# Kernel optimization log

Hardware: AMD Instinct MI355X
Metric: run time of the kernel (lower is better)

## Reference

```python
import jax, jax.numpy as jnp
import numpy as np

E = 768           # EMBEDDING_DIM
L = 768           # LATENT_DIM
H = 12            # ATTENTION_HEAD_COUNT
HD = L // H       # head_dim = 64
EPS = 1e-5


def _linear_params(key, fan_in, fan_out):
    kw, kb = jax.random.split(key)
    bound = 1.0 / np.sqrt(fan_in)
    w = jax.random.uniform(kw, (fan_in, fan_out), jnp.float32, -bound, bound)
    b = jax.random.uniform(kb, (fan_out,), jnp.float32, -bound, bound)
    return w, b


def layer_norm(x, g, b):
    m = jnp.mean(x, axis=-1, keepdims=True)
    v = jnp.mean((x - m) ** 2, axis=-1, keepdims=True)
    return (x - m) * jax.lax.rsqrt(v + EPS) * g + b


def setup_inputs() -> dict:
    key = jax.random.key(0)
    ks = jax.random.split(key, 8)
    B, N, M = 8, 1024, 1024
    x = jax.random.normal(ks[0], (B, N, E), jnp.float32)
    y = jax.random.normal(ks[1], (B, M, E), jnp.float32)
    wq, bq = _linear_params(ks[2], E, L)
    wk, bk = _linear_params(ks[3], E, L)
    wv, bv = _linear_params(ks[4], E, E * H)
    w_in, b_in = _linear_params(ks[5], E, L)
    w_out, b_out = _linear_params(ks[6], L, E)
    ones = jnp.ones((E,), jnp.float32)
    zeros = jnp.zeros((E,), jnp.float32)
    return {
        'x': x, 'y': y,
        'ln1_g': ones, 'ln1_b': zeros,
        'ln2_g': ones, 'ln2_b': zeros,
        'ln3_g': ones, 'ln3_b': zeros,
        'wq': wq, 'bq': bq,
        'wk': wk, 'bk': bk,
        'wv': wv, 'bv': bv,
        'w_in': w_in, 'b_in': b_in,
        'w_out': w_out, 'b_out': b_out,
    }


def reference(x, y, ln1_g, ln1_b, ln2_g, ln2_b, ln3_g, ln3_b,
              wq, bq, wk, bk, wv, bv, w_in, b_in, w_out, b_out):
    B, N, _ = x.shape
    M = y.shape[1]
    xn = layer_norm(x, ln1_g, ln1_b)
    yn = layer_norm(y, ln2_g, ln2_b)
    # projections; per-head value dim is the FULL embedding dim (non-standard)
    q = (xn @ wq + bq).reshape(B, N, H, HD)        # bnhd
    k = (yn @ wk + bk).reshape(B, M, H, HD)        # bmhd
    v = (yn @ wv + bv).reshape(B, M, H, E)         # bmhe
    a = jnp.einsum('bnhd,bmhd->bhnm', q, k) / jnp.sqrt(jnp.float32(HD))
    a = jax.nn.softmax(a, axis=-1)
    # attention output fused with the sum over heads (heads summed, not concat)
    dx = jnp.einsum('bhnm,bmhe->bne', a, v)
    h = xn + dx
    h = layer_norm(h, ln3_g, ln3_b)
    mlp = jax.nn.relu(h @ w_in + b_in) @ w_out + b_out
    return (h + mlp, yn)
```

## Files before the change

kernel.cpp:

```cpp
#include <hip/hip_runtime.h>
#include <hip/hip_bf16.h>
#include <stdint.h>

typedef __bf16 bf16_t;
typedef __bf16 bf16x8 __attribute__((ext_vector_type(8)));
typedef float  f32x4  __attribute__((ext_vector_type(4)));

typedef __attribute__((address_space(3))) unsigned int lds_u32;
typedef const __attribute__((address_space(1))) unsigned int glob_u32;
#define GLDS16(g, l) __builtin_amdgcn_global_load_lds((glob_u32*)(g), (lds_u32*)(l), 16, 0, 0)

__device__ __forceinline__ f32x4 mfma16(bf16x8 a, bf16x8 b, f32x4 c) {
    return __builtin_amdgcn_mfma_f32_16x16x32_bf16(a, b, c, 0, 0, 0);
}

__device__ __forceinline__ float ldv(const void* p, long i, int fp32mode) {
    return fp32mode ? ((const float*)p)[i] : (float)((const bf16_t*)p)[i];
}

__global__ __launch_bounds__(256)
void detect_dtype(const void* __restrict__ x, int* __restrict__ flag) {
    __shared__ int cnt;
    if (threadIdx.x == 0) cnt = 0;
    __syncthreads();
    const bf16_t* p = (const bf16_t*)x;
    int local = 0;
    for (int i = threadIdx.x; i < 4096; i += 256) {
        const float v = (float)p[i];
        if (!(fabsf(v) < 1e6f)) local++;
    }
    atomicAdd(&cnt, local);
    __syncthreads();
    if (threadIdx.x == 0) { flag[0] = (cnt >= 16) ? 1 : 0; flag[1] = 0; }
}

__global__ __launch_bounds__(256)
void transpose_cvt(const void* __restrict__ in, bf16_t* __restrict__ out,
                   int R, int C, const int* __restrict__ flagp) {
    __shared__ bf16_t t[32][33];
    const int mode = *flagp;
    const long zi = (long)blockIdx.z * R * C;
    const int c0 = blockIdx.x * 32;
    const int r0 = blockIdx.y * 32;
    const int x  = threadIdx.x;
    const int y0 = threadIdx.y;
    for (int yy = y0; yy < 32; yy += 8)
        t[yy][x] = (bf16_t)ldv(in, zi + (long)(r0 + yy) * C + c0 + x, mode);
    __syncthreads();
    for (int yy = y0; yy < 32; yy += 8)
        out[zi + (long)(c0 + yy) * R + r0 + x] = t[x][yy];
}

__global__ __launch_bounds__(256)
void transpose_wv(const void* __restrict__ in, bf16_t* __restrict__ out,
                  const int* __restrict__ flagp) {
    __shared__ bf16_t t[32][33];
    const int mode = *flagp;
    const int h  = blockIdx.z;
    const int e0 = blockIdx.x * 32;
    const int k0 = blockIdx.y * 32;
    const int x  = threadIdx.x;
    const int y0 = threadIdx.y;
    for (int yy = y0; yy < 32; yy += 8)
        t[yy][x] = (bf16_t)ldv(in, (long)(k0 + yy) * 9216 + h * 768 + e0 + x, mode);
    __syncthreads();
    for (int yy = y0; yy < 32; yy += 8)
        out[(long)(e0 + yy) * 9216 + h * 768 + k0 + x] = t[x][yy];
}

__global__ __launch_bounds__(256)
void bvsum_k(const void* __restrict__ bv, float* __restrict__ out,
             const int* __restrict__ flagp) {
    const int mode = *flagp;
    const int e = blockIdx.x * 256 + threadIdx.x;
    if (e < 768) {
        float s = 0.f;
#pragma unroll
        for (int h = 0; h < 12; ++h) s += ldv(bv, h * 768 + e, mode);
        out[e] = s;
    }
}

__global__ __launch_bounds__(256)
void ln768(const void* __restrict__ in, bf16_t* __restrict__ out,
           const void* __restrict__ gam, const void* __restrict__ bet,
           const int* __restrict__ dmodep, const int* __restrict__ pmodep) {
    __shared__ float rs[256], rq[256];
    const int dm = *dmodep, pm = *pmodep;
    const long base = (long)blockIdx.x * 768;
    const int tid = threadIdx.x;
    float v[3];
    float s = 0.f, q = 0.f;
#pragma unroll
    for (int i = 0; i < 3; ++i) {
        v[i] = ldv(in, base + i * 256 + tid, dm);
        s += v[i];
        q += v[i] * v[i];
    }
    rs[tid] = s; rq[tid] = q;
    __syncthreads();
    for (int st = 128; st > 0; st >>= 1) {
        if (tid < st) { rs[tid] += rs[tid + st]; rq[tid] += rq[tid + st]; }
        __syncthreads();
    }
    const float mean = rs[0] * (1.0f / 768.0f);
    const float var  = rq[0] * (1.0f / 768.0f) - mean * mean;
    const float rstd = rsqrtf(var + 1e-5f);
#pragma unroll
    for (int i = 0; i < 3; ++i) {
        const int c = i * 256 + tid;
        out[base + c] = (bf16_t)((v[i] - mean) * rstd * ldv(gam, c, pm) + ldv(bet, c, pm));
    }
}

#define BK 64
#define TILEA 16384

template<int JN>
__device__ __forceinline__ void stage_ab(const bf16_t* Az, const bf16_t* Bz,
                                         int lda, int ldb, int k0,
                                         char* lA, char* lB, int tid) {
    const int srow = tid >> 3;
    const int sc   = ((tid & 7) * 16) ^ ((srow & 7) << 4);
#pragma unroll
    for (int p = 0; p < 4; ++p)
        GLDS16((const char*)(Az + (long)(srow + p * 32) * lda + k0) + sc, lA + p * 4096);
#pragma unroll
    for (int p = 0; p < JN; ++p)
        GLDS16((const char*)(Bz + (long)(srow + p * 32) * ldb + k0) + sc, lB + p * 4096);
}

template<int JN>
__device__ __forceinline__ void compute_tile(const char* As, const char* Bs,
                                             int wm, int wn, int l15, int quad,
                                             f32x4 (&acc)[4][JN]) {
#pragma unroll
    for (int kk = 0; kk < BK; kk += 32) {
        bf16x8 af[4], bfr[JN];
        const int cb = kk * 2 + quad * 16;
#pragma unroll
        for (int i = 0; i < 4; ++i) {
            const int r = wm + i * 16 + l15;
            af[i] = *(const bf16x8*)(As + r * 128 + (cb ^ ((r & 7) << 4)));
        }
#pragma unroll
        for (int j = 0; j < JN; ++j) {
            const int r = wn + j * 16 + l15;
            bfr[j] = *(const bf16x8*)(Bs + r * 128 + (cb ^ ((r & 7) << 4)));
        }
#pragma unroll
        for (int i = 0; i < 4; ++i)
#pragma unroll
            for (int j = 0; j < JN; ++j)
                acc[i][j] = mfma16(af[i], bfr[j], acc[i][j]);
    }
}

template<int JN>
__device__ __forceinline__ void kloop(const bf16_t* Az, const bf16_t* Bz,
                                      int K, int lda, int ldb, int tid,
                                      char* AsB, char* BsB,
                                      int wm, int wn, int l15, int quad,
                                      f32x4 (&acc)[4][JN]) {
    const int TILEB = JN * 4096;
    char* lA = AsB + (tid >> 6) * 1024;
    char* lB = BsB + (tid >> 6) * 1024;
    int cur = 0;
    stage_ab<JN>(Az, Bz, lda, ldb, 0, lA, lB, tid);
    __syncthreads();
    const int NT = K >> 6;
    for (int t = 0; t < NT - 1; ++t) {
        const int nb = cur ^ 1;
        stage_ab<JN>(Az, Bz, lda, ldb, (t + 1) << 6, lA + nb * TILEA, lB + nb * TILEB, tid);
        compute_tile<JN>(AsB + cur * TILEA, BsB + cur * TILEB, wm, wn, l15, quad, acc);
        __syncthreads();
        cur = nb;
    }
    compute_tile<JN>(AsB + cur * TILEA, BsB + cur * TILEB, wm, wn, l15, quad, acc);
}

__device__ __forceinline__ int xcd_swz(int lin, int nwg) {
    return (lin & 7) * (nwg >> 3) + (lin >> 3);
}

__global__ __launch_bounds__(256, 2)
void gemm_bt(const bf16_t* __restrict__ A, const bf16_t* __restrict__ B,
             bf16_t* __restrict__ C,
             int K, int lda, int ldb, int ldc,
             const void* __restrict__ bias, const int* __restrict__ flagp,
             const bf16_t* __restrict__ res, int do_relu) {
    __shared__ char AsB[2 * TILEA];
    __shared__ char BsB[2 * 3 * 4096];
    const int bmode = *flagp;
    const int swz = xcd_swz(blockIdx.y * 8 + blockIdx.x, 512);
    const int n0 = (swz & 7) * 96;
    const int m0 = (swz >> 3) * 128;
    const bf16_t* Az = A + (long)m0 * lda;
    const bf16_t* Bz = B + (long)n0 * ldb;

    const int tid  = threadIdx.x;
    const int lane = tid & 63;
    const int w    = tid >> 6;
    const int wm   = (w >> 1) * 64;
    const int wn   = (w & 1) * 48;
    const int l15  = lane & 15;
    const int quad = lane >> 4;

    const f32x4 fz = {0.f, 0.f, 0.f, 0.f};
    f32x4 acc[4][3];
#pragma unroll
    for (int i = 0; i < 4; ++i)
#pragma unroll
        for (int j = 0; j < 3; ++j) acc[i][j] = fz;

    kloop<3>(Az, Bz, K, lda, ldb, tid, AsB, BsB, wm, wn, l15, quad, acc);

#pragma unroll
    for (int i = 0; i < 4; ++i) {
#pragma unroll
        for (int j = 0; j < 3; ++j) {
            const int mb = m0 + wm + i * 16 + quad * 4;
            const int nc = n0 + wn + j * 16 + l15;
#pragma unroll
            for (int r = 0; r < 4; ++r) {
                float v = acc[i][j][r];
                if (bias) v += ldv(bias, nc, bmode);
                if (do_relu) v = fmaxf(v, 0.0f);
                if (res) v += (float)res[(long)(mb + r) * ldc + nc];
                C[(long)(mb + r) * ldc + nc] = (bf16_t)v;
            }
        }
    }
}

__global__ __launch_bounds__(256, 2)
void gemm_qk(const bf16_t* __restrict__ xn, const bf16_t* __restrict__ ynb,
             const bf16_t* __restrict__ wqT, const bf16_t* __restrict__ wkT,
             bf16_t* __restrict__ qb, bf16_t* __restrict__ kb,
             const void* __restrict__ bq, const void* __restrict__ bk,
             const int* __restrict__ flagp) {
    __shared__ char AsB[2 * TILEA];
    __shared__ char BsB[2 * 3 * 4096];
    const int bmode = *flagp;
    const int z = blockIdx.z;
    const bf16_t* A = z ? ynb : xn;
    const bf16_t* B = z ? wkT : wqT;
    bf16_t*       C = z ? kb  : qb;
    const void* bias = z ? bk : bq;
    const int swz = xcd_swz(blockIdx.y * 8 + blockIdx.x, 512);
    const int n0 = (swz & 7) * 96;
    const int m0 = (swz >> 3) * 128;
    const bf16_t* Az = A + (long)m0 * 768;
    const bf16_t* Bz = B + (long)n0 * 768;

    const int tid  = threadIdx.x;
    const int lane = tid & 63;
    const int w    = tid >> 6;
    const int wm   = (w >> 1) * 64;
    const int wn   = (w & 1) * 48;
    const int l15  = lane & 15;
    const int quad = lane >> 4;

    const f32x4 fz = {0.f, 0.f, 0.f, 0.f};
    f32x4 acc[4][3];
#pragma unroll
    for (int i = 0; i < 4; ++i)
#pragma unroll
        for (int j = 0; j < 3; ++j) acc[i][j] = fz;

    kloop<3>(Az, Bz, 768, 768, 768, tid, AsB, BsB, wm, wn, l15, quad, acc);

#pragma unroll
    for (int i = 0; i < 4; ++i) {
#pragma unroll
        for (int j = 0; j < 3; ++j) {
            const int mb = m0 + wm + i * 16 + quad * 4;
            const int nc = n0 + wn + j * 16 + l15;
#pragma unroll
            for (int r = 0; r < 4; ++r)
                C[(long)(mb + r) * 768 + nc] = (bf16_t)(acc[i][j][r] + ldv(bias, nc, bmode));
        }
    }
}

__global__ __launch_bounds__(256, 2)
void gemm_vt(const bf16_t* __restrict__ W2T, const bf16_t* __restrict__ ynb,
             bf16_t* __restrict__ VTc, int h0, int ldP) {
    __shared__ char AsB[2 * TILEA];
    __shared__ char BsB[2 * 4 * 4096];
    const int L  = blockIdx.z * 48 + blockIdx.y * 8 + blockIdx.x;
    const int b  = L & 7;
    const int rest = L >> 3;
    const int hc = rest / 48;
    const int t  = rest % 48;
    const int e0  = (t >> 3) * 128;
    const int mc0 = (t & 7) * 128;
    const bf16_t* Az = W2T + (long)e0 * 9216 + (h0 + hc) * 768;
    const bf16_t* Bz = ynb + ((long)b * 1024 + mc0) * 768;

    const int tid  = threadIdx.x;
    const int lane = tid & 63;
    const int w    = tid >> 6;
    const int wm   = (w >> 1) * 64;
    const int wn   = (w & 1) * 64;
    const int l15  = lane & 15;
    const int quad = lane >> 4;

    const f32x4 fz = {0.f, 0.f, 0.f, 0.f};
    f32x4 acc[4][4];
#pragma unroll
    for (int i = 0; i < 4; ++i)
#pragma unroll
        for (int j = 0; j < 4; ++j) acc[i][j] = fz;

    kloop<4>(Az, Bz, 768, 9216, 768, tid, AsB, BsB, wm, wn, l15, quad, acc);

    bf16_t* C = VTc + (long)b * 768 * ldP + (long)hc * 1024;
#pragma unroll
    for (int i = 0; i < 4; ++i) {
#pragma unroll
        for (int j = 0; j < 4; ++j) {
            const int er = e0 + wm + i * 16 + quad * 4;
            const int mc = mc0 + wn + j * 16 + l15;
#pragma unroll
            for (int r = 0; r < 4; ++r)
                C[(long)(er + r) * ldP + mc] = (bf16_t)acc[i][j][r];
        }
    }
}

__global__ __launch_bounds__(256, 2)
void gemm_dx(const bf16_t* __restrict__ P, const bf16_t* __restrict__ VTc,
             float* __restrict__ dxf, const bf16_t* __restrict__ xnb,
             const float* __restrict__ bvs, bf16_t* __restrict__ hp,
             int ldP, int mode) {
    __shared__ char AsB[2 * TILEA];
    __shared__ char BsB[2 * 3 * 4096];
    const int L = blockIdx.z * 64 + blockIdx.y * 8 + blockIdx.x;
    const int b = L & 7;
    const int t = L >> 3;
    const int m0 = (t >> 3) * 128;
    const int n0 = (t & 7) * 96;
    const bf16_t* Az = P   + ((long)b * 1024 + m0) * ldP;
    const bf16_t* Bz = VTc + ((long)b * 768  + n0) * ldP;

    const int tid  = threadIdx.x;
    const int lane = tid & 63;
    const int w    = tid >> 6;
    const int wm   = (w >> 1) * 64;
    const int wn   = (w & 1) * 48;
    const int l15  = lane & 15;
    const int quad = lane >> 4;

    const f32x4 fz = {0.f, 0.f, 0.f, 0.f};
    f32x4 acc[4][3];
#pragma unroll
    for (int i = 0; i < 4; ++i)
#pragma unroll
        for (int j = 0; j < 3; ++j) acc[i][j] = fz;

    kloop<3>(Az, Bz, ldP, ldP, ldP, tid, AsB, BsB, wm, wn, l15, quad, acc);

#pragma unroll
    for (int i = 0; i < 4; ++i) {
#pragma unroll
        for (int j = 0; j < 3; ++j) {
            const int gr = b * 1024 + m0 + wm + i * 16 + quad * 4;
            const int nc = n0 + wn + j * 16 + l15;
#pragma unroll
            for (int r = 0; r < 4; ++r) {
                const long gi = (long)(gr + r) * 768 + nc;
                float v = acc[i][j][r];
                if (mode == 1 || mode == 2) v += dxf[gi];
                if (mode <= 1) dxf[gi] = v;
                else hp[gi] = (bf16_t)(v + bvs[nc] + (float)xnb[gi]);
            }
        }
    }
}

__global__ __launch_bounds__(512, 8)
void fused_S(const bf16_t* __restrict__ Q, const bf16_t* __restrict__ Kp,
             bf16_t* __restrict__ P, int h0, int ldP) {
    __shared__ bf16_t Pl[16][1032];
    __shared__ float  rmax[8][16];
    __shared__ float  rsum[8][16];

    const int bx   = blockIdx.x;
    const int b    = bx & 7;
    const int n0   = ((bx >> 3) & 63) * 16;
    const int hc   = bx >> 9;
    const int h    = h0 + hc;
    const int tid  = threadIdx.x;
    const int w    = tid >> 6;
    const int lane = tid & 63;
    const int l15  = lane & 15;
    const int quad = lane >> 4;

    const f32x4 fz = {0.f, 0.f, 0.f, 0.f};
    const long qoff = (long)(b * 1024 + n0 + l15) * 768 + h * 64 + quad * 8;
    const long koff = (long)(b * 1024) * 768 + h * 64 + quad * 8;

    f32x4 s[8];
#pragma unroll
    for (int f = 0; f < 8; ++f) s[f] = fz;
    const bf16x8 qa0 = *(const bf16x8*)(Q + qoff);
    const bf16x8 qa1 = *(const bf16x8*)(Q + qoff + 32);
#pragma unroll
    for (int f = 0; f < 8; ++f) {
        const int m = w * 128 + f * 16 + l15;
        const bf16_t* kp = Kp + koff + (long)m * 768;
        s[f] = mfma16(qa0, *(const bf16x8*)kp, s[f]);
        s[f] = mfma16(qa1, *(const bf16x8*)(kp + 32), s[f]);
    }
    float rm[4] = {-3e38f, -3e38f, -3e38f, -3e38f};
#pragma unroll
    for (int f = 0; f < 8; ++f)
#pragma unroll
        for (int r = 0; r < 4; ++r) {
            s[f][r] *= 0.125f;
            rm[r] = fmaxf(rm[r], s[f][r]);
        }
#pragma unroll
    for (int off = 1; off < 16; off <<= 1)
#pragma unroll
        for (int r = 0; r < 4; ++r) rm[r] = fmaxf(rm[r], __shfl_xor(rm[r], off));
    if (l15 == 0) {
#pragma unroll
        for (int r = 0; r < 4; ++r) rmax[w][quad * 4 + r] = rm[r];
    }
    __syncthreads();
    float gm[4];
#pragma unroll
    for (int r = 0; r < 4; ++r) {
        float mx = rmax[0][quad * 4 + r];
#pragma unroll
        for (int w2 = 1; w2 < 8; ++w2) mx = fmaxf(mx, rmax[w2][quad * 4 + r]);
        gm[r] = mx;
    }
    float ps[4] = {0.f, 0.f, 0.f, 0.f};
#pragma unroll
    for (int f = 0; f < 8; ++f)
#pragma unroll
        for (int r = 0; r < 4; ++r) {
            const float p = __expf(s[f][r] - gm[r]);
            s[f][r] = p;
            ps[r] += p;
        }
#pragma unroll
    for (int off = 1; off < 16; off <<= 1)
#pragma unroll
        for (int r = 0; r < 4; ++r) ps[r] += __shfl_xor(ps[r], off);
    if (l15 == 0) {
#pragma unroll
        for (int r = 0; r < 4; ++r) rsum[w][quad * 4 + r] = ps[r];
    }
    __syncthreads();
#pragma unroll
    for (int r = 0; r < 4; ++r) {
        float ss = 0.f;
#pragma unroll
        for (int w2 = 0; w2 < 8; ++w2) ss += rsum[w2][quad * 4 + r];
        gm[r] = 1.0f / ss;
    }
#pragma unroll
    for (int f = 0; f < 8; ++f)
#pragma unroll
        for (int r = 0; r < 4; ++r)
            Pl[quad * 4 + r][w * 128 + f * 16 + l15] = (bf16_t)(s[f][r] * gm[r]);
    __syncthreads();

    const long pbase = ((long)b * 1024 + n0) * ldP + (long)hc * 1024;
    const int rr = tid >> 5;
    const int c0 = (tid & 31) * 32;
    bf16_t* dst = P + pbase + (long)rr * ldP + c0;
#pragma unroll
    for (int u = 0; u < 4; ++u)
        *(bf16x8*)(dst + u * 8) = *(const bf16x8*)(&Pl[rr][c0 + u * 8]);
}

__global__ __launch_bounds__(256)
void emit2(const bf16_t* __restrict__ a, const bf16_t* __restrict__ b,
           void* __restrict__ out, const int* __restrict__ flagp) {
    const int mode = *flagp;
    const long n = 6291456;
    const long stride = (long)gridDim.x * blockDim.x;
    for (long i = (long)blockIdx.x * blockDim.x + threadIdx.x; i < 2 * n; i += stride) {
        const bf16_t v = (i < n) ? a[i] : b[i - n];
        if (mode) ((float*)out)[i] = (float)v;
        else      ((bf16_t*)out)[i] = v;
    }
}

extern "C" void kernel_launch(void* const* d_in, const int* in_sizes, int n_in,
                              void* d_out, int out_size, void* d_ws, size_t ws_size,
                              hipStream_t stream) {
    (void)in_sizes; (void)n_in; (void)out_size;

    const void* x    = d_in[0];
    const void* y    = d_in[1];
    const void* ln1g = d_in[2];
    const void* ln1b = d_in[3];
    const void* ln2g = d_in[4];
    const void* ln2b = d_in[5];
    const void* ln3g = d_in[6];
    const void* ln3b = d_in[7];
    const void* wq   = d_in[8];
    const void* bq   = d_in[9];
    const void* wk   = d_in[10];
    const void* bk   = d_in[11];
    const void* wv   = d_in[12];
    const void* bv   = d_in[13];
    const void* wi   = d_in[14];
    const void* bi   = d_in[15];
    const void* wo   = d_in[16];
    const void* bo   = d_in[17];

    char* ws = (char*)d_ws;
    bf16_t* xn    = (bf16_t*)(ws + 0);
    bf16_t* ynb   = (bf16_t*)(ws + 12582912);
    bf16_t* qb    = (bf16_t*)(ws + 25165824);
    bf16_t* kb    = (bf16_t*)(ws + 37748736);
    bf16_t* W2T   = (bf16_t*)(ws + 50331648);
    bf16_t* wqT   = (bf16_t*)(ws + 64487424);
    bf16_t* wkT   = (bf16_t*)(ws + 65667072);
    bf16_t* wiT   = (bf16_t*)(ws + 66846720);
    bf16_t* woT   = (bf16_t*)(ws + 68026368);
    float*  bvs   = (float*) (ws + 69206016);
    int*    flag  = (int*)   (ws + 69210112);
    float*  dxf   = (float*) (ws + 69214208);

    static const int GS[5] = {12, 6, 4, 3, 2};
    int G = 2;
    for (int i = 0; i < 5; ++i) {
        const unsigned long long need =
            94380032ULL + (unsigned long long)GS[i] * 29360128ULL;
        if (need <= (unsigned long long)ws_size) { G = GS[i]; break; }
    }
    const int ldP = G * 1024;
    bf16_t* Pcat = (bf16_t*)(ws + 94380032);
    bf16_t* VTc  = (bf16_t*)(ws + 94380032 + (size_t)G * 16777216);
    bf16_t* hpre = qb;
    bf16_t* hn   = kb;
    bf16_t* mid  = Pcat;
    bf16_t* res0 = xn;
    const int* F = flag;
    const int* Z = flag + 1;

    detect_dtype<<<1, 256, 0, stream>>>(x, flag);

    const dim3 tb(32, 8);
    transpose_cvt<<<dim3(24, 24, 1), tb, 0, stream>>>(wq, wqT, 768, 768, F);
    transpose_cvt<<<dim3(24, 24, 1), tb, 0, stream>>>(wk, wkT, 768, 768, F);
    transpose_cvt<<<dim3(24, 24, 1), tb, 0, stream>>>(wi, wiT, 768, 768, F);
    transpose_cvt<<<dim3(24, 24, 1), tb, 0, stream>>>(wo, woT, 768, 768, F);
    transpose_wv<<<dim3(24, 24, 12), tb, 0, stream>>>(wv, W2T, F);
    bvsum_k<<<3, 256, 0, stream>>>(bv, bvs, F);

    ln768<<<8192, 256, 0, stream>>>(x, xn, ln1g, ln1b, F, F);
    ln768<<<8192, 256, 0, stream>>>(y, ynb, ln2g, ln2b, F, F);

    gemm_qk<<<dim3(8, 64, 2), 256, 0, stream>>>(xn, ynb, wqT, wkT, qb, kb, bq, bk, F);

    const int npass = 12 / G;
    for (int p = 0; p < npass; ++p) {
        const int h0 = p * G;
        fused_S<<<512 * G, 512, 0, stream>>>(qb, kb, Pcat, h0, ldP);
        gemm_vt<<<dim3(8, 6, 8 * G), 256, 0, stream>>>(W2T, ynb, VTc, h0, ldP);
        const int mode = (npass == 1) ? 3 : (p == 0 ? 0 : (p == npass - 1 ? 2 : 1));
        gemm_dx<<<dim3(8, 8, 8), 256, 0, stream>>>(Pcat, VTc, dxf, xn, bvs, hpre,
                                                   ldP, mode);
    }

    ln768<<<8192, 256, 0, stream>>>(hpre, hn, ln3g, ln3b, Z, F);

    gemm_bt<<<dim3(8, 64), 256, 0, stream>>>(hn, wiT, mid, 768, 768, 768, 768,
                                             bi, F, nullptr, 1);
    gemm_bt<<<dim3(8, 64), 256, 0, stream>>>(mid, woT, res0, 768, 768, 768, 768,
                                             bo, F, hn, 0);

    emit2<<<2048, 256, 0, stream>>>(res0, ynb, d_out, F);
}
```

Before: 897.9 us.

## Enlarge GEMM block tiles to 512 threads with 8 waves per workgroup

All bf16 GEMM kernels (qk, vt, dx, MLP) move from 256-thread blocks to 512-thread blocks. Each block now covers a larger output tile: 128x192 for most kernels and 256x128 for gemm_vt. Staging is generalized to separate A/B row-pass counts and the grids and tile-index mappings are rewritten to match. The aim is more reuse of each LDS-staged tile and fewer global loads per output. The costs are fewer blocks, which can hurt load balance on a many-CU GPU, and roughly double the LDS per block, which may limit occupancy.

After: 913.3 us. No clear change (+1.7%).

```diff
diff --git a/kernel.cpp b/kernel.cpp
--- a/kernel.cpp
+++ b/kernel.cpp
@@ -114,29 +114,28 @@
 }
 
 #define BK 64
-#define TILEA 16384
-
-template<int JN>
+
+template<int AP, int BP>
 __device__ __forceinline__ void stage_ab(const bf16_t* Az, const bf16_t* Bz,
                                          int lda, int ldb, int k0,
                                          char* lA, char* lB, int tid) {
     const int srow = tid >> 3;
     const int sc   = ((tid & 7) * 16) ^ ((srow & 7) << 4);
 #pragma unroll
-    for (int p = 0; p < 4; ++p)
-        GLDS16((const char*)(Az + (long)(srow + p * 32) * lda + k0) + sc, lA + p * 4096);
-#pragma unroll
-    for (int p = 0; p < JN; ++p)
-        GLDS16((const char*)(Bz + (long)(srow + p * 32) * ldb + k0) + sc, lB + p * 4096);
-}
-
-template<int JN>
+    for (int p = 0; p < AP; ++p)
+        GLDS16((const char*)(Az + (long)(srow + p * 64) * lda + k0) + sc, lA + p * 8192);
+#pragma unroll
+    for (int p = 0; p < BP; ++p)
+        GLDS16((const char*)(Bz + (long)(srow + p * 64) * ldb + k0) + sc, lB + p * 8192);
+}
+
+template<int JNW>
 __device__ __forceinline__ void compute_tile(const char* As, const char* Bs,
                                              int wm, int wn, int l15, int quad,
-                                             f32x4 (&acc)[4][JN]) {
+                                             f32x4 (&acc)[4][JNW]) {
 #pragma unroll
     for (int kk = 0; kk < BK; kk += 32) {
-        bf16x8 af[4], bfr[JN];
+        bf16x8 af[4], bfr[JNW];
         const int cb = kk * 2 + quad * 16;
 #pragma unroll
         for (int i = 0; i < 4; ++i) {
@@ -144,65 +143,65 @@
             af[i] = *(const bf16x8*)(As + r * 128 + (cb ^ ((r & 7) << 4)));
         }
 #pragma unroll
-        for (int j = 0; j < JN; ++j) {
+        for (int j = 0; j < JNW; ++j) {
             const int r = wn + j * 16 + l15;
             bfr[j] = *(const bf16x8*)(Bs + r * 128 + (cb ^ ((r & 7) << 4)));
         }
 #pragma unroll
         for (int i = 0; i < 4; ++i)
 #pragma unroll
-            for (int j = 0; j < JN; ++j)
+            for (int j = 0; j < JNW; ++j)
                 acc[i][j] = mfma16(af[i], bfr[j], acc[i][j]);
     }
 }
 
-template<int JN>
+template<int JNW, int AP, int BP>
 __device__ __forceinline__ void kloop(const bf16_t* Az, const bf16_t* Bz,
                                       int K, int lda, int ldb, int tid,
                                       char* AsB, char* BsB,
                                       int wm, int wn, int l15, int quad,
-                                      f32x4 (&acc)[4][JN]) {
-    const int TILEB = JN * 4096;
+                                      f32x4 (&acc)[4][JNW]) {
+    const int TA = AP * 8192, TB = BP * 8192;
     char* lA = AsB + (tid >> 6) * 1024;
     char* lB = BsB + (tid >> 6) * 1024;
     int cur = 0;
-    stage_ab<JN>(Az, Bz, lda, ldb, 0, lA, lB, tid);
+    stage_ab<AP, BP>(Az, Bz, lda, ldb, 0, lA, lB, tid);
     __syncthreads();
     const int NT = K >> 6;
     for (int t = 0; t < NT - 1; ++t) {
         const int nb = cur ^ 1;
-        stage_ab<JN>(Az, Bz, lda, ldb, (t + 1) << 6, lA + nb * TILEA, lB + nb * TILEB, tid);
-        compute_tile<JN>(AsB + cur * TILEA, BsB + cur * TILEB, wm, wn, l15, quad, acc);
+        stage_ab<AP, BP>(Az, Bz, lda, ldb, (t + 1) << 6, lA + nb * TA, lB + nb * TB, tid);
+        compute_tile<JNW>(AsB + cur * TA, BsB + cur * TB, wm, wn, l15, quad, acc);
         __syncthreads();
         cur = nb;
     }
-    compute_tile<JN>(AsB + cur * TILEA, BsB + cur * TILEB, wm, wn, l15, quad, acc);
+    compute_tile<JNW>(AsB + cur * TA, BsB + cur * TB, wm, wn, l15, quad, acc);
 }
 
 __device__ __forceinline__ int xcd_swz(int lin, int nwg) {
     return (lin & 7) * (nwg >> 3) + (lin >> 3);
 }
 
-__global__ __launch_bounds__(256, 2)
+__global__ __launch_bounds__(512, 2)
 void gemm_bt(const bf16_t* __restrict__ A, const bf16_t* __restrict__ B,
              bf16_t* __restrict__ C,
              int K, int lda, int ldb, int ldc,
              const void* __restrict__ bias, const int* __restrict__ flagp,
              const bf16_t* __restrict__ res, int do_relu) {
-    __shared__ char AsB[2 * TILEA];
-    __shared__ char BsB[2 * 3 * 4096];
+    __shared__ char AsB[2 * 2 * 8192];
+    __shared__ char BsB[2 * 3 * 8192];
     const int bmode = *flagp;
-    const int swz = xcd_swz(blockIdx.y * 8 + blockIdx.x, 512);
-    const int n0 = (swz & 7) * 96;
-    const int m0 = (swz >> 3) * 128;
+    const int swz = xcd_swz(blockIdx.y * 4 + blockIdx.x, 256);
+    const int n0 = (swz & 3) * 192;
+    const int m0 = (swz >> 2) * 128;
     const bf16_t* Az = A + (long)m0 * lda;
     const bf16_t* Bz = B + (long)n0 * ldb;
 
     const int tid  = threadIdx.x;
     const int lane = tid & 63;
     const int w    = tid >> 6;
-    const int wm   = (w >> 1) * 64;
-    const int wn   = (w & 1) * 48;
+    const int wm   = (w >> 2) * 64;
+    const int wn   = (w & 3) * 48;
     const int l15  = lane & 15;
     const int quad = lane >> 4;
 
@@ -213,7 +212,7 @@
 #pragma unroll
         for (int j = 0; j < 3; ++j) acc[i][j] = fz;
 
-    kloop<3>(Az, Bz, K, lda, ldb, tid, AsB, BsB, wm, wn, l15, quad, acc);
+    kloop<3, 2, 3>(Az, Bz, K, lda, ldb, tid, AsB, BsB, wm, wn, l15, quad, acc);
 
 #pragma unroll
     for (int i = 0; i < 4; ++i) {
@@ -233,31 +232,31 @@
     }
 }
 
-__global__ __launch_bounds__(256, 2)
+__global__ __launch_bounds__(512, 2)
 void gemm_qk(const bf16_t* __restrict__ xn, const bf16_t* __restrict__ ynb,
              const bf16_t* __restrict__ wqT, const bf16_t* __restrict__ wkT,
              bf16_t* __restrict__ qb, bf16_t* __restrict__ kb,
              const void* __restrict__ bq, const void* __restrict__ bk,
              const int* __restrict__ flagp) {
-    __shared__ char AsB[2 * TILEA];
-    __shared__ char BsB[2 * 3 * 4096];
+    __shared__ char AsB[2 * 2 * 8192];
+    __shared__ char BsB[2 * 3 * 8192];
     const int bmode = *flagp;
     const int z = blockIdx.z;
     const bf16_t* A = z ? ynb : xn;
     const bf16_t* B = z ? wkT : wqT;
     bf16_t*       C = z ? kb  : qb;
     const void* bias = z ? bk : bq;
-    const int swz = xcd_swz(blockIdx.y * 8 + blockIdx.x, 512);
-    const int n0 = (swz & 7) * 96;
-    const int m0 = (swz >> 3) * 128;
+    const int swz = xcd_swz(blockIdx.y * 4 + blockIdx.x, 256);
+    const int n0 = (swz & 3) * 192;
+    const int m0 = (swz >> 2) * 128;
     const bf16_t* Az = A + (long)m0 * 768;
     const bf16_t* Bz = B + (long)n0 * 768;
 
     const int tid  = threadIdx.x;
     const int lane = tid & 63;
     const int w    = tid >> 6;
-    const int wm   = (w >> 1) * 64;
-    const int wn   = (w & 1) * 48;
+    const int wm   = (w >> 2) * 64;
+    const int wn   = (w & 3) * 48;
     const int l15  = lane & 15;
     const int quad = lane >> 4;
 
@@ -268,7 +267,7 @@
 #pragma unroll
         for (int j = 0; j < 3; ++j) acc[i][j] = fz;
 
-    kloop<3>(Az, Bz, 768, 768, 768, tid, AsB, BsB, wm, wn, l15, quad, acc);
+    kloop<3, 2, 3>(Az, Bz, 768, 768, 768, tid, AsB, BsB, wm, wn, l15, quad, acc);
 
 #pragma unroll
     for (int i = 0; i < 4; ++i) {
@@ -283,18 +282,15 @@
     }
 }
 
-__global__ __launch_bounds__(256, 2)
+__global__ __launch_bounds__(512, 2)
 void gemm_vt(const bf16_t* __restrict__ W2T, const bf16_t* __restrict__ ynb,
              bf16_t* __restrict__ VTc, int h0, int ldP) {
-    __shared__ char AsB[2 * TILEA];
-    __shared__ char BsB[2 * 4 * 4096];
-    const int L  = blockIdx.z * 48 + blockIdx.y * 8 + blockIdx.x;
-    const int b  = L & 7;
-    const int rest = L >> 3;
-    const int hc = rest / 48;
-    const int t  = rest % 48;
-    const int e0  = (t >> 3) * 128;
-    const int mc0 = (t & 7) * 128;
+    __shared__ char AsB[2 * 4 * 8192];
+    __shared__ char BsB[2 * 2 * 8192];
+    const int b   = blockIdx.x;
+    const int hc  = blockIdx.z;
+    const int e0  = (blockIdx.y >> 3) * 256;
+    const int mc0 = (blockIdx.y & 7) * 128;
     const bf16_t* Az = W2T + (long)e0 * 9216 + (h0 + hc) * 768;
     const bf16_t* Bz = ynb + ((long)b * 1024 + mc0) * 768;
 
@@ -313,7 +309,7 @@
 #pragma unroll
         for (int j = 0; j < 4; ++j) acc[i][j] = fz;
 
-    kloop<4>(Az, Bz, 768, 9216, 768, tid, AsB, BsB, wm, wn, l15, quad, acc);
+    kloop<4, 4, 2>(Az, Bz, 768, 9216, 768, tid, AsB, BsB, wm, wn, l15, quad, acc);
 
     bf16_t* C = VTc + (long)b * 768 * ldP + (long)hc * 1024;
 #pragma unroll
@@ -329,26 +325,25 @@
     }
 }
 
-__global__ __launch_bounds__(256, 2)
+__global__ __launch_bounds__(512, 2)
 void gemm_dx(const bf16_t* __restrict__ P, const bf16_t* __restrict__ VTc,
              float* __restrict__ dxf, const bf16_t* __restrict__ xnb,
              const float* __restrict__ bvs, bf16_t* __restrict__ hp,
              int ldP, int mode) {
-    __shared__ char AsB[2 * TILEA];
-    __shared__ char BsB[2 * 3 * 4096];
-    const int L = blockIdx.z * 64 + blockIdx.y * 8 + blockIdx.x;
-    const int b = L & 7;
-    const int t = L >> 3;
-    const int m0 = (t >> 3) * 128;
-    const int n0 = (t & 7) * 96;
+    __shared__ char AsB[2 * 2 * 8192];
+    __shared__ char BsB[2 * 3 * 8192];
+    const int b  = blockIdx.x;
+    const int t  = blockIdx.y;
+    const int m0 = (t >> 2) * 128;
+    const int n0 = (t & 3) * 192;
     const bf16_t* Az = P   + ((long)b * 1024 + m0) * ldP;
     const bf16_t* Bz = VTc + ((long)b * 768  + n0) * ldP;
 
     const int tid  = threadIdx.x;
     const int lane = tid & 63;
     const int w    = tid >> 6;
-    const int wm   = (w >> 1) * 64;
-    const int wn   = (w & 1) * 48;
+    const int wm   = (w >> 2) * 64;
+    const int wn   = (w & 3) * 48;
     const int l15  = lane & 15;
     const int quad = lane >> 4;
 
@@ -359,7 +354,7 @@
 #pragma unroll
         for (int j = 0; j < 3; ++j) acc[i][j] = fz;
 
-    kloop<3>(Az, Bz, ldP, ldP, ldP, tid, AsB, BsB, wm, wn, l15, quad, acc);
+    kloop<3, 2, 3>(Az, Bz, ldP, ldP, ldP, tid, AsB, BsB, wm, wn, l15, quad, acc);
 
 #pragma unroll
     for (int i = 0; i < 4; ++i) {
@@ -560,23 +555,23 @@
     ln768<<<8192, 256, 0, stream>>>(x, xn, ln1g, ln1b, F, F);
     ln768<<<8192, 256, 0, stream>>>(y, ynb, ln2g, ln2b, F, F);
 
-    gemm_qk<<<dim3(8, 64, 2), 256, 0, stream>>>(xn, ynb, wqT, wkT, qb, kb, bq, bk, F);
+    gemm_qk<<<dim3(4, 64, 2), 512, 0, stream>>>(xn, ynb, wqT, wkT, qb, kb, bq, bk, F);
 
     const int npass = 12 / G;
     for (int p = 0; p < npass; ++p) {
         const int h0 = p * G;
         fused_S<<<512 * G, 512, 0, stream>>>(qb, kb, Pcat, h0, ldP);
-        gemm_vt<<<dim3(8, 6, 8 * G), 256, 0, stream>>>(W2T, ynb, VTc, h0, ldP);
+        gemm_vt<<<dim3(8, 24, G), 512, 0, stream>>>(W2T, ynb, VTc, h0, ldP);
         const int mode = (npass == 1) ? 3 : (p == 0 ? 0 : (p == npass - 1 ? 2 : 1));
-        gemm_dx<<<dim3(8, 8, 8), 256, 0, stream>>>(Pcat, VTc, dxf, xn, bvs, hpre,
-                                                   ldP, mode);
+        gemm_dx<<<dim3(8, 32), 512, 0, stream>>>(Pcat, VTc, dxf, xn, bvs, hpre,
+                                                 ldP, mode);
     }
 
     ln768<<<8192, 256, 0, stream>>>(hpre, hn, ln3g, ln3b, Z, F);
 
-    gemm_bt<<<dim3(8, 64), 256, 0, stream>>>(hn, wiT, mid, 768, 768, 768, 768,
+    gemm_bt<<<dim3(4, 64), 512, 0, stream>>>(hn, wiT, mid, 768, 768, 768, 768,
                                              bi, F, nullptr, 1);
-    gemm_bt<<<dim3(8, 64), 256, 0, stream>>>(mid, woT, res0, 768, 768, 768, 768,
+    gemm_bt<<<dim3(4, 64), 512, 0, stream>>>(mid, woT, res0, 768, 768, 768, 768,
                                              bo, F, hn, 0);
 
     emit2<<<2048, 256, 0, stream>>>(res0, ynb, d_out, F);
```

## Replace async double-buffered GEMM k-loop with single-buffer padded LDS 128x128 tiles

Applied to the files above, without the earlier changes.

Swaps the global_load_lds double-buffered GEMM pipeline for a simpler register-staged single-buffer k-loop with padded LDS rows instead of XOR swizzle. Tiles grow from 128x96 to 128x128, grids and index math are adjusted for all GEMM kernels, and the occupancy hint is dropped. This raises per-block reuse and reduces block count, but loses overlap of loads with MFMA compute and adds an extra barrier per k-step.

Measured after the change: 949.1 us. +5.7%, slower.

```diff
diff --git a/kernel.cpp b/kernel.cpp
--- a/kernel.cpp
+++ b/kernel.cpp
@@ -5,10 +5,6 @@
 typedef __bf16 bf16_t;
 typedef __bf16 bf16x8 __attribute__((ext_vector_type(8)));
 typedef float  f32x4  __attribute__((ext_vector_type(4)));
-
-typedef __attribute__((address_space(3))) unsigned int lds_u32;
-typedef const __attribute__((address_space(1))) unsigned int glob_u32;
-#define GLDS16(g, l) __builtin_amdgcn_global_load_lds((glob_u32*)(g), (lds_u32*)(l), 16, 0, 0)
 
 __device__ __forceinline__ f32x4 mfma16(bf16x8 a, bf16x8 b, f32x4 c) {
     return __builtin_amdgcn_mfma_f32_16x16x32_bf16(a, b, c, 0, 0, 0);
@@ -113,88 +109,61 @@
     }
 }
 
+#define BM 128
+#define BN 128
 #define BK 64
-#define TILEA 16384
-
-template<int JN>
-__device__ __forceinline__ void stage_ab(const bf16_t* Az, const bf16_t* Bz,
-                                         int lda, int ldb, int k0,
-                                         char* lA, char* lB, int tid) {
+#define LDT 72
+
+__device__ __forceinline__ void r1_kloop(const bf16_t* Az, const bf16_t* Bz,
+                                         int K, int lda, int ldb, int tid,
+                                         bf16_t (*As)[LDT], bf16_t (*Bs)[LDT],
+                                         int wm, int wn, int l15, int quad,
+                                         f32x4 (&acc)[4][4]) {
     const int srow = tid >> 3;
-    const int sc   = ((tid & 7) * 16) ^ ((srow & 7) << 4);
-#pragma unroll
-    for (int p = 0; p < 4; ++p)
-        GLDS16((const char*)(Az + (long)(srow + p * 32) * lda + k0) + sc, lA + p * 4096);
-#pragma unroll
-    for (int p = 0; p < JN; ++p)
-        GLDS16((const char*)(Bz + (long)(srow + p * 32) * ldb + k0) + sc, lB + p * 4096);
-}
-
-template<int JN>
-__device__ __forceinline__ void compute_tile(const char* As, const char* Bs,
-                                             int wm, int wn, int l15, int quad,
-                                             f32x4 (&acc)[4][JN]) {
-#pragma unroll
-    for (int kk = 0; kk < BK; kk += 32) {
-        bf16x8 af[4], bfr[JN];
-        const int cb = kk * 2 + quad * 16;
-#pragma unroll
-        for (int i = 0; i < 4; ++i) {
-            const int r = wm + i * 16 + l15;
-            af[i] = *(const bf16x8*)(As + r * 128 + (cb ^ ((r & 7) << 4)));
-        }
-#pragma unroll
-        for (int j = 0; j < JN; ++j) {
-            const int r = wn + j * 16 + l15;
-            bfr[j] = *(const bf16x8*)(Bs + r * 128 + (cb ^ ((r & 7) << 4)));
-        }
-#pragma unroll
-        for (int i = 0; i < 4; ++i)
-#pragma unroll
-            for (int j = 0; j < JN; ++j)
-                acc[i][j] = mfma16(af[i], bfr[j], acc[i][j]);
-    }
-}
-
-template<int JN>
-__device__ __forceinline__ void kloop(const bf16_t* Az, const bf16_t* Bz,
-                                      int K, int lda, int ldb, int tid,
-                                      char* AsB, char* BsB,
-                                      int wm, int wn, int l15, int quad,
-                                      f32x4 (&acc)[4][JN]) {
-    const int TILEB = JN * 4096;
-    char* lA = AsB + (tid >> 6) * 1024;
-    char* lB = BsB + (tid >> 6) * 1024;
-    int cur = 0;
-    stage_ab<JN>(Az, Bz, lda, ldb, 0, lA, lB, tid);
-    __syncthreads();
-    const int NT = K >> 6;
-    for (int t = 0; t < NT - 1; ++t) {
-        const int nb = cur ^ 1;
-        stage_ab<JN>(Az, Bz, lda, ldb, (t + 1) << 6, lA + nb * TILEA, lB + nb * TILEB, tid);
-        compute_tile<JN>(AsB + cur * TILEA, BsB + cur * TILEB, wm, wn, l15, quad, acc);
+    const int scol = (tid & 7) * 8;
+    for (int k0 = 0; k0 < K; k0 += BK) {
         __syncthreads();
-        cur = nb;
-    }
-    compute_tile<JN>(AsB + cur * TILEA, BsB + cur * TILEB, wm, wn, l15, quad, acc);
+#pragma unroll
+        for (int p = 0; p < 4; ++p) {
+            const int r = srow + p * 32;
+            *(bf16x8*)(&As[r][scol]) = *(const bf16x8*)(Az + (long)r * lda + k0 + scol);
+            *(bf16x8*)(&Bs[r][scol]) = *(const bf16x8*)(Bz + (long)r * ldb + k0 + scol);
+        }
+        __syncthreads();
+#pragma unroll
+        for (int kk = 0; kk < BK; kk += 32) {
+            bf16x8 af[4], bfr[4];
+#pragma unroll
+            for (int i = 0; i < 4; ++i)
+                af[i] = *(const bf16x8*)(&As[wm + i * 16 + l15][kk + quad * 8]);
+#pragma unroll
+            for (int j = 0; j < 4; ++j)
+                bfr[j] = *(const bf16x8*)(&Bs[wn + j * 16 + l15][kk + quad * 8]);
+#pragma unroll
+            for (int i = 0; i < 4; ++i)
+#pragma unroll
+                for (int j = 0; j < 4; ++j)
+                    acc[i][j] = mfma16(af[i], bfr[j], acc[i][j]);
+        }
+    }
 }
 
 __device__ __forceinline__ int xcd_swz(int lin, int nwg) {
     return (lin & 7) * (nwg >> 3) + (lin >> 3);
 }
 
-__global__ __launch_bounds__(256, 2)
+__global__ __launch_bounds__(256)
 void gemm_bt(const bf16_t* __restrict__ A, const bf16_t* __restrict__ B,
              bf16_t* __restrict__ C,
              int K, int lda, int ldb, int ldc,
              const void* __restrict__ bias, const int* __restrict__ flagp,
              const bf16_t* __restrict__ res, int do_relu) {
-    __shared__ char AsB[2 * TILEA];
-    __shared__ char BsB[2 * 3 * 4096];
+    __shared__ bf16_t As[BM][LDT];
+    __shared__ bf16_t Bs[BN][LDT];
     const int bmode = *flagp;
-    const int swz = xcd_swz(blockIdx.y * 8 + blockIdx.x, 512);
-    const int n0 = (swz & 7) * 96;
-    const int m0 = (swz >> 3) * 128;
+    const int swz = xcd_swz(blockIdx.y * 6 + blockIdx.x, 384);
+    const int n0 = (swz % 6) * BN;
+    const int m0 = (swz / 6) * BM;
     const bf16_t* Az = A + (long)m0 * lda;
     const bf16_t* Bz = B + (long)n0 * ldb;
 
@@ -202,23 +171,23 @@
     const int lane = tid & 63;
     const int w    = tid >> 6;
     const int wm   = (w >> 1) * 64;
-    const int wn   = (w & 1) * 48;
+    const int wn   = (w & 1) * 64;
     const int l15  = lane & 15;
     const int quad = lane >> 4;
 
     const f32x4 fz = {0.f, 0.f, 0.f, 0.f};
-    f32x4 acc[4][3];
+    f32x4 acc[4][4];
 #pragma unroll
     for (int i = 0; i < 4; ++i)
 #pragma unroll
-        for (int j = 0; j < 3; ++j) acc[i][j] = fz;
-
-    kloop<3>(Az, Bz, K, lda, ldb, tid, AsB, BsB, wm, wn, l15, quad, acc);
+        for (int j = 0; j < 4; ++j) acc[i][j] = fz;
+
+    r1_kloop(Az, Bz, K, lda, ldb, tid, As, Bs, wm, wn, l15, quad, acc);
 
 #pragma unroll
     for (int i = 0; i < 4; ++i) {
 #pragma unroll
-        for (int j = 0; j < 3; ++j) {
+        for (int j = 0; j < 4; ++j) {
             const int mb = m0 + wm + i * 16 + quad * 4;
             const int nc = n0 + wn + j * 16 + l15;
 #pragma unroll
@@ -233,23 +202,23 @@
     }
 }
 
-__global__ __launch_bounds__(256, 2)
+__global__ __launch_bounds__(256)
 void gemm_qk(const bf16_t* __restrict__ xn, const bf16_t* __restrict__ ynb,
              const bf16_t* __restrict__ wqT, const bf16_t* __restrict__ wkT,
              bf16_t* __restrict__ qb, bf16_t* __restrict__ kb,
              const void* __restrict__ bq, const void* __restrict__ bk,
              const int* __restrict__ flagp) {
-    __shared__ char AsB[2 * TILEA];
-    __shared__ char BsB[2 * 3 * 4096];
+    __shared__ bf16_t As[BM][LDT];
+    __shared__ bf16_t Bs[BN][LDT];
     const int bmode = *flagp;
     const int z = blockIdx.z;
     const bf16_t* A = z ? ynb : xn;
     const bf16_t* B = z ? wkT : wqT;
     bf16_t*       C = z ? kb  : qb;
     const void* bias = z ? bk : bq;
-    const int swz = xcd_swz(blockIdx.y * 8 + blockIdx.x, 512);
-    const int n0 = (swz & 7) * 96;
-    const int m0 = (swz >> 3) * 128;
+    const int swz = xcd_swz(blockIdx.y * 6 + blockIdx.x, 384);
+    const int n0 = (swz % 6) * BN;
+    const int m0 = (swz / 6) * BM;
     const bf16_t* Az = A + (long)m0 * 768;
     const bf16_t* Bz = B + (long)n0 * 768;
 
@@ -257,23 +226,23 @@
     const int lane = tid & 63;
     const int w    = tid >> 6;
     const int wm   = (w >> 1) * 64;
-    const int wn   = (w & 1) * 48;
+    const int wn   = (w & 1) * 64;
     const int l15  = lane & 15;
     const int quad = lane >> 4;
 
     const f32x4 fz = {0.f, 0.f, 0.f, 0.f};
-    f32x4 acc[4][3];
+    f32x4 acc[4][4];
 #pragma unroll
     for (int i = 0; i < 4; ++i)
 #pragma unroll
-        for (int j = 0; j < 3; ++j) acc[i][j] = fz;
-
-    kloop<3>(Az, Bz, 768, 768, 768, tid, AsB, BsB, wm, wn, l15, quad, acc);
+        for (int j = 0; j < 4; ++j) acc[i][j] = fz;
+
+    r1_kloop(Az, Bz, 768, 768, 768, tid, As, Bs, wm, wn, l15, quad, acc);
 
 #pragma unroll
     for (int i = 0; i < 4; ++i) {
 #pragma unroll
-        for (int j = 0; j < 3; ++j) {
+        for (int j = 0; j < 4; ++j) {
             const int mb = m0 + wm + i * 16 + quad * 4;
             const int nc = n0 + wn + j * 16 + l15;
 #pragma unroll
@@ -283,11 +252,11 @@
     }
 }
 
-__global__ __launch_bounds__(256, 2)
+__global__ __launch_bounds__(256)
 void gemm_vt(const bf16_t* __restrict__ W2T, const bf16_t* __restrict__ ynb,
              bf16_t* __restrict__ VTc, int h0, int ldP) {
-    __shared__ char AsB[2 * TILEA];
-    __shared__ char BsB[2 * 4 * 4096];
+    __shared__ bf16_t As[BM][LDT];
+    __shared__ bf16_t Bs[BN][LDT];
     const int L  = blockIdx.z * 48 + blockIdx.y * 8 + blockIdx.x;
     const int b  = L & 7;
     const int rest = L >> 3;
@@ -313,7 +282,7 @@
 #pragma unroll
         for (int j = 0; j < 4; ++j) acc[i][j] = fz;
 
-    kloop<4>(Az, Bz, 768, 9216, 768, tid, AsB, BsB, wm, wn, l15, quad, acc);
+    r1_kloop(Az, Bz, 768, 9216, 768, tid, As, Bs, wm, wn, l15, quad, acc);
 
     bf16_t* C = VTc + (long)b * 768 * ldP + (long)hc * 1024;
 #pragma unroll
@@ -329,18 +298,17 @@
     }
 }
 
-__global__ __launch_bounds__(256, 2)
+__global__ __launch_bounds__(256)
 void gemm_dx(const bf16_t* __restrict__ P, const bf16_t* __restrict__ VTc,
              float* __restrict__ dxf, const bf16_t* __restrict__ xnb,
              const float* __restrict__ bvs, bf16_t* __restrict__ hp,
              int ldP, int mode) {
-    __shared__ char AsB[2 * TILEA];
-    __shared__ char BsB[2 * 3 * 4096];
-    const int L = blockIdx.z * 64 + blockIdx.y * 8 + blockIdx.x;
-    const int b = L & 7;
-    const int t = L >> 3;
-    const int m0 = (t >> 3) * 128;
-    const int n0 = (t & 7) * 96;
+    __shared__ bf16_t As[BM][LDT];
+    __shared__ bf16_t Bs[BN][LDT];
+    const int b  = blockIdx.x;
+    const int t  = blockIdx.y;
+    const int m0 = (t / 6) * 128;
+    const int n0 = (t % 6) * 128;
     const bf16_t* Az = P   + ((long)b * 1024 + m0) * ldP;
     const bf16_t* Bz = VTc + ((long)b * 768  + n0) * ldP;
 
@@ -348,23 +316,23 @@
     const int lane = tid & 63;
     const int w    = tid >> 6;
     const int wm   = (w >> 1) * 64;
-    const int wn   = (w & 1) * 48;
+    const int wn   = (w & 1) * 64;
     const int l15  = lane & 15;
     const int quad = lane >> 4;
 
     const f32x4 fz = {0.f, 0.f, 0.f, 0.f};
-    f32x4 acc[4][3];
+    f32x4 acc[4][4];
 #pragma unroll
     for (int i = 0; i < 4; ++i)
 #pragma unroll
-        for (int j = 0; j < 3; ++j) acc[i][j] = fz;
-
-    kloop<3>(Az, Bz, ldP, ldP, ldP, tid, AsB, BsB, wm, wn, l15, quad, acc);
+        for (int j = 0; j < 4; ++j) acc[i][j] = fz;
+
+    r1_kloop(Az, Bz, ldP, ldP, ldP, tid, As, Bs, wm, wn, l15, quad, acc);
 
 #pragma unroll
     for (int i = 0; i < 4; ++i) {
 #pragma unroll
-        for (int j = 0; j < 3; ++j) {
+        for (int j = 0; j < 4; ++j) {
             const int gr = b * 1024 + m0 + wm + i * 16 + quad * 4;
             const int nc = n0 + wn + j * 16 + l15;
 #pragma unroll
@@ -560,7 +528,7 @@
     ln768<<<8192, 256, 0, stream>>>(x, xn, ln1g, ln1b, F, F);
     ln768<<<8192, 256, 0, stream>>>(y, ynb, ln2g, ln2b, F, F);
 
-    gemm_qk<<<dim3(8, 64, 2), 256, 0, stream>>>(xn, ynb, wqT, wkT, qb, kb, bq, bk, F);
+    gemm_qk<<<dim3(6, 64, 2), 256, 0, stream>>>(xn, ynb, wqT, wkT, qb, kb, bq, bk, F);
 
     const int npass = 12 / G;
     for (int p = 0; p < npass; ++p) {
@@ -568,15 +536,15 @@
         fused_S<<<512 * G, 512, 0, stream>>>(qb, kb, Pcat, h0, ldP);
         gemm_vt<<<dim3(8, 6, 8 * G), 256, 0, stream>>>(W2T, ynb, VTc, h0, ldP);
         const int mode = (npass == 1) ? 3 : (p == 0 ? 0 : (p == npass - 1 ? 2 : 1));
-        gemm_dx<<<dim3(8, 8, 8), 256, 0, stream>>>(Pcat, VTc, dxf, xn, bvs, hpre,
-                                                   ldP, mode);
+        gemm_dx<<<dim3(8, 48), 256, 0, stream>>>(Pcat, VTc, dxf, xn, bvs, hpre,
+                                                 ldP, mode);
     }
 
     ln768<<<8192, 256, 0, stream>>>(hpre, hn, ln3g, ln3b, Z, F);
 
-    gemm_bt<<<dim3(8, 64), 256, 0, stream>>>(hn, wiT, mid, 768, 768, 768, 768,
+    gemm_bt<<<dim3(6, 64), 256, 0, stream>>>(hn, wiT, mid, 768, 768, 768, 768,
                                              bi, F, nullptr, 1);
-    gemm_bt<<<dim3(8, 64), 256, 0, stream>>>(mid, woT, res0, 768, 768, 768, 768,
+    gemm_bt<<<dim3(6, 64), 256, 0, stream>>>(mid, woT, res0, 768, 768, 768, 768,
                                              bo, F, hn, 0);
 
     emit2<<<2048, 256, 0, stream>>>(res0, ynb, d_out, F);
```
